# Kernel optimization log

Hardware: AMD Instinct MI355X
Metric: run time of the kernel (lower is better)

## Reference

```python
import jax, jax.numpy as jnp
import numpy as np

N = 100000   # nodes
E = 1600000  # edges (avg degree 16)
IN_F = 256
OUT_F = 128


def setup_inputs() -> dict:
    key = jax.random.key(0)
    k1, k2, k3, k4, k5, k6 = jax.random.split(key, 6)
    std = 1.0 / (OUT_F ** 0.5)
    return {
        "x": jax.random.normal(k1, (N, IN_F), dtype=jnp.float32),
        "weight": jax.random.uniform(k2, (IN_F, OUT_F), dtype=jnp.float32, minval=-std, maxval=std),
        "bias": jax.random.uniform(k3, (OUT_F,), dtype=jnp.float32, minval=-std, maxval=std),
        "edge_weight": jax.random.uniform(k4, (E,), dtype=jnp.float32),
        "row": jax.random.randint(k5, (E,), 0, N, dtype=jnp.int32),
        "col": jax.random.randint(k6, (E,), 0, N, dtype=jnp.int32),
    }


def reference(x, weight, bias, edge_weight, row, col):
    # support = x @ W : dense GEMM [N, in] x [in, out]
    support = jnp.matmul(x, weight)
    # spmm(adj, support): gather source-node rows, scale by edge value,
    # scatter-add into destination rows (COO SpMM).
    msgs = support[col] * edge_weight[:, None]          # [E, out]
    aggregated = jax.ops.segment_sum(msgs, row, num_segments=N)  # [N, out]
    return aggregated + bias
```

## Files before the change

kernel.cpp:

```cpp
#include <hip/hip_runtime.h>

#define N_NODES 100000
#define IN_F 256
#define OUT_F 128

#define BKT_SHIFT 6
#define BKT_SIZE (1 << BKT_SHIFT)
#define NBKT ((N_NODES + BKT_SIZE - 1) / BKT_SIZE)
#define SLAB_CAP 2048
#define CHUNK 8192

#define WS_SUP 0
#define WS_SLAB 25600000
#define WS_BSWZ 51300000
#define WS_BCUR 51400000
#define WS_NEEDED 65200016

typedef __attribute__((ext_vector_type(8))) short short8;
typedef __attribute__((ext_vector_type(4))) float f32x4;
typedef __attribute__((ext_vector_type(2))) float f32x2;

__device__ __forceinline__ unsigned short f2bf(float f) {
  unsigned u = __float_as_uint(f);
  unsigned r = (u + 0x7fffu + ((u >> 16) & 1u)) >> 16;
  return (unsigned short)r;
}

__global__ __launch_bounds__(256) void prep_bswz_kernel(
    const float* __restrict__ w, unsigned short* __restrict__ bswz,
    int* __restrict__ bcur) {
  const int tid = blockIdx.x * 256 + threadIdx.x;
  if (tid < NBKT) bcur[tid] = 0;
  const int j = tid & 7;
  const int lane = (tid >> 3) & 63;
  const int nt = (tid >> 9) & 7;
  const int ks = tid >> 12;
  const int k = ks * 32 + ((lane >> 4) * 8) + j;
  const int n = nt * 16 + (lane & 15);
  bswz[tid] = f2bf(w[k * OUT_F + n]);
}

__global__ __launch_bounds__(512, 4) void gemm_mfma_kernel(
    const float* __restrict__ x, const unsigned short* __restrict__ bswz,
    unsigned short* __restrict__ supb) {
  __shared__ unsigned short lb[32768];

  const int t = threadIdx.x;
  {
    const int4* src = (const int4*)bswz;
    int4* dst = (int4*)lb;
#pragma unroll
    for (int i = 0; i < 8; ++i) dst[t + i * 512] = src[t + i * 512];
  }
  __syncthreads();

  const int w = t >> 6;
  const int lane = t & 63;
  const int quad = lane >> 4;
  const int m16 = lane & 15;

  const int row = blockIdx.x * 128 + w * 16 + m16;
  const int rc = row < N_NODES ? row : N_NODES - 1;
  const float* ap = x + (long long)rc * IN_F + quad * 8;
  const short8* bb = (const short8*)lb + lane;

  f32x4 acc[8];
#pragma unroll
  for (int nt = 0; nt < 8; ++nt) acc[nt] = (f32x4){0.f, 0.f, 0.f, 0.f};

  float4 A0[8], A1[8];
#pragma unroll
  for (int p = 0; p < 6; ++p) {
    A0[p] = *(const float4*)(ap + p * 32);
    A1[p] = *(const float4*)(ap + p * 32 + 4);
  }

#pragma unroll
  for (int ks = 0; ks < 8; ++ks) {
    if (ks + 6 < 8) {
      A0[ks + 6] = *(const float4*)(ap + (ks + 6) * 32);
      A1[ks + 6] = *(const float4*)(ap + (ks + 6) * 32 + 4);
    }
    short8 af;
    af[0] = f2bf(A0[ks].x); af[1] = f2bf(A0[ks].y);
    af[2] = f2bf(A0[ks].z); af[3] = f2bf(A0[ks].w);
    af[4] = f2bf(A1[ks].x); af[5] = f2bf(A1[ks].y);
    af[6] = f2bf(A1[ks].z); af[7] = f2bf(A1[ks].w);
#pragma unroll
    for (int nt = 0; nt < 8; ++nt) {
      const short8 bf = bb[(ks * 8 + nt) * 64];
      acc[nt] = __builtin_amdgcn_mfma_f32_16x16x32_bf16(af, bf, acc[nt], 0, 0, 0);
    }
  }

  const int rowbase = blockIdx.x * 128 + w * 16 + quad * 4;
#pragma unroll
  for (int nt = 0; nt < 8; ++nt) {
#pragma unroll
    for (int r = 0; r < 4; ++r) {
      const int gr = rowbase + r;
      if (gr < N_NODES)
        supb[(long long)gr * OUT_F + nt * 16 + m16] = f2bf(acc[nt][r]);
    }
  }
}

__global__ __launch_bounds__(1024) void bucket_fill_kernel(
    const int* __restrict__ row, const int* __restrict__ col,
    const float* __restrict__ ew, int* __restrict__ bcur,
    int2* __restrict__ slab, int E) {
  __shared__ int lcnt[2048];
  __shared__ int sc[2048];
  __shared__ int outb[2048];
  __shared__ int2 stage[CHUNK];
  __shared__ unsigned short bid[CHUNK];

  const int t = threadIdx.x;
  const int e0 = blockIdx.x * CHUNK;
  lcnt[t] = 0;
  lcnt[t + 1024] = 0;
  __syncthreads();

  int myb[8];
  int rank[8];
  int2 pk[8];
#pragma unroll
  for (int k = 0; k < 8; ++k) {
    const int e = e0 + k * 1024 + t;
    myb[k] = -1;
    if (e < E) {
      const int r = row[e];
      const int c = col[e];
      const float wv = ew[e];
      const int b = r >> BKT_SHIFT;
      myb[k] = b;
      pk[k] = make_int2(c | ((r & (BKT_SIZE - 1)) << 17), __float_as_int(wv));
      rank[k] = atomicAdd(&lcnt[b], 1);
    }
  }
  __syncthreads();

  const int v0 = lcnt[t];
  const int v1 = lcnt[t + 1024];
  sc[t] = v0;
  sc[t + 1024] = v1;
  __syncthreads();
  for (int off = 1; off < 1024; off <<= 1) {
    const int w0 = (t >= off) ? sc[t - off] : 0;
    const int w1 = (t >= off) ? sc[1024 + t - off] : 0;
    __syncthreads();
    sc[t] += w0;
    sc[1024 + t] += w1;
    __syncthreads();
  }
  const int tot0 = sc[1023];
  __syncthreads();
  sc[1024 + t] += tot0;
  __syncthreads();
  const int ex0 = sc[t] - v0;
  const int ex1 = sc[1024 + t] - v1;
  if (v0) outb[t] = atomicAdd(&bcur[t], v0);
  if (t + 1024 < NBKT && v1) outb[t + 1024] = atomicAdd(&bcur[t + 1024], v1);
  __syncthreads();
  sc[t] = ex0;
  sc[t + 1024] = ex1;
  __syncthreads();

#pragma unroll
  for (int k = 0; k < 8; ++k) {
    if (myb[k] >= 0) {
      const int p = sc[myb[k]] + rank[k];
      stage[p] = pk[k];
      bid[p] = (unsigned short)myb[k];
    }
  }
  __syncthreads();

  const int total = min(CHUNK, E - e0);
  for (int i = t; i < total; i += 1024) {
    const int b = bid[i];
    const int rel = outb[b] + (i - sc[b]);
    if (rel < SLAB_CAP) slab[(long long)b * SLAB_CAP + rel] = stage[i];
  }
}

__global__ __launch_bounds__(256) void node_gather_kernel(
    const unsigned short* __restrict__ supb, const int2* __restrict__ slab,
    const int* __restrict__ bcur, const float* __restrict__ bias,
    float* __restrict__ out) {
  __shared__ int2 eS[SLAB_CAP];
  __shared__ int hist[BKT_SIZE];
  __shared__ int sbase[BKT_SIZE];
  __shared__ int cur[BKT_SIZE];

  const int t = threadIdx.x;
  const int bk = blockIdx.x;
  const long long sb = (long long)bk * SLAB_CAP;
  int n = bcur[bk];
  n = n > SLAB_CAP ? SLAB_CAP : n;

  const int w = t >> 6;
  const int lane = t & 63;
  const unsigned short* sp = supb + lane * 2;
  const float2 bv = *(const float2*)(bias + lane * 2);

  if (t < BKT_SIZE) hist[t] = 0;
  __syncthreads();
  for (int i = t; i < n; i += 256)
    atomicAdd(&hist[(slab[sb + i].x >> 17) & (BKT_SIZE - 1)], 1);
  __syncthreads();
  int v = 0;
  if (t < BKT_SIZE) { v = hist[t]; sbase[t] = v; }
  __syncthreads();
  for (int off = 1; off < BKT_SIZE; off <<= 1) {
    int add = 0;
    if (t < BKT_SIZE && t >= off) add = sbase[t - off];
    __syncthreads();
    if (t < BKT_SIZE) sbase[t] += add;
    __syncthreads();
  }
  if (t < BKT_SIZE) { sbase[t] -= v; cur[t] = sbase[t]; }
  __syncthreads();
  for (int i = t; i < n; i += 256) {
    const int2 e = slab[sb + i];
    const int lr = (e.x >> 17) & (BKT_SIZE - 1);
    eS[atomicAdd(&cur[lr], 1)] = e;
  }
  __syncthreads();

  for (int k = 0; k < 16; ++k) {
    const int lr0 = w * 16 + k;
    const int node = (bk << BKT_SHIFT) + lr0;
    if (node >= N_NODES) break;
    const int s = sbase[lr0];
    const int e_end = s + hist[lr0];
    float a0 = 0.f, a1 = 0.f, b0 = 0.f, b1 = 0.f;
    float c0 = 0.f, c1 = 0.f, d0 = 0.f, d1 = 0.f;
    float p0 = 0.f, p1 = 0.f, q0 = 0.f, q1 = 0.f;
    float r0 = 0.f, r1 = 0.f, s0 = 0.f, s1 = 0.f;
    int j = s;
    for (; j + 8 <= e_end; j += 8) {
      const int2 E0 = eS[j];     const int2 E1 = eS[j + 1];
      const int2 E2 = eS[j + 2]; const int2 E3 = eS[j + 3];
      const int2 E4 = eS[j + 4]; const int2 E5 = eS[j + 5];
      const int2 E6 = eS[j + 6]; const int2 E7 = eS[j + 7];
      const unsigned u0 = *(const unsigned*)(sp + (long long)(E0.x & 0x1FFFF) * OUT_F);
      const unsigned u1 = *(const unsigned*)(sp + (long long)(E1.x & 0x1FFFF) * OUT_F);
      const unsigned u2 = *(const unsigned*)(sp + (long long)(E2.x & 0x1FFFF) * OUT_F);
      const unsigned u3 = *(const unsigned*)(sp + (long long)(E3.x & 0x1FFFF) * OUT_F);
      const unsigned u4 = *(const unsigned*)(sp + (long long)(E4.x & 0x1FFFF) * OUT_F);
      const unsigned u5 = *(const unsigned*)(sp + (long long)(E5.x & 0x1FFFF) * OUT_F);
      const unsigned u6 = *(const unsigned*)(sp + (long long)(E6.x & 0x1FFFF) * OUT_F);
      const unsigned u7 = *(const unsigned*)(sp + (long long)(E7.x & 0x1FFFF) * OUT_F);
      a0 = fmaf(__uint_as_float(u0 << 16), __int_as_float(E0.y), a0);
      a1 = fmaf(__uint_as_float(u0 & 0xffff0000u), __int_as_float(E0.y), a1);
      b0 = fmaf(__uint_as_float(u1 << 16), __int_as_float(E1.y), b0);
      b1 = fmaf(__uint_as_float(u1 & 0xffff0000u), __int_as_float(E1.y), b1);
      c0 = fmaf(__uint_as_float(u2 << 16), __int_as_float(E2.y), c0);
      c1 = fmaf(__uint_as_float(u2 & 0xffff0000u), __int_as_float(E2.y), c1);
      d0 = fmaf(__uint_as_float(u3 << 16), __int_as_float(E3.y), d0);
      d1 = fmaf(__uint_as_float(u3 & 0xffff0000u), __int_as_float(E3.y), d1);
      p0 = fmaf(__uint_as_float(u4 << 16), __int_as_float(E4.y), p0);
      p1 = fmaf(__uint_as_float(u4 & 0xffff0000u), __int_as_float(E4.y), p1);
      q0 = fmaf(__uint_as_float(u5 << 16), __int_as_float(E5.y), q0);
      q1 = fmaf(__uint_as_float(u5 & 0xffff0000u), __int_as_float(E5.y), q1);
      r0 = fmaf(__uint_as_float(u6 << 16), __int_as_float(E6.y), r0);
      r1 = fmaf(__uint_as_float(u6 & 0xffff0000u), __int_as_float(E6.y), r1);
      s0 = fmaf(__uint_as_float(u7 << 16), __int_as_float(E7.y), s0);
      s1 = fmaf(__uint_as_float(u7 & 0xffff0000u), __int_as_float(E7.y), s1);
    }
    for (; j + 2 <= e_end; j += 2) {
      const int2 E0 = eS[j];
      const int2 E1 = eS[j + 1];
      const unsigned u0 = *(const unsigned*)(sp + (long long)(E0.x & 0x1FFFF) * OUT_F);
      const unsigned u1 = *(const unsigned*)(sp + (long long)(E1.x & 0x1FFFF) * OUT_F);
      a0 = fmaf(__uint_as_float(u0 << 16), __int_as_float(E0.y), a0);
      a1 = fmaf(__uint_as_float(u0 & 0xffff0000u), __int_as_float(E0.y), a1);
      b0 = fmaf(__uint_as_float(u1 << 16), __int_as_float(E1.y), b0);
      b1 = fmaf(__uint_as_float(u1 & 0xffff0000u), __int_as_float(E1.y), b1);
    }
    if (j < e_end) {
      const int2 E0 = eS[j];
      const unsigned u0 = *(const unsigned*)(sp + (long long)(E0.x & 0x1FFFF) * OUT_F);
      a0 = fmaf(__uint_as_float(u0 << 16), __int_as_float(E0.y), a0);
      a1 = fmaf(__uint_as_float(u0 & 0xffff0000u), __int_as_float(E0.y), a1);
    }
    const f32x2 vv = {a0 + b0 + c0 + d0 + p0 + q0 + r0 + s0 + bv.x,
                      a1 + b1 + c1 + d1 + p1 + q1 + r1 + s1 + bv.y};
    __builtin_nontemporal_store(vv, (f32x2*)(out + (long long)node * OUT_F + lane * 2));
  }
}

__global__ __launch_bounds__(256) void bias_init_kernel(
    float* __restrict__ out, const float* __restrict__ bias) {
  const int t = blockIdx.x * blockDim.x + threadIdx.x;
  const int idx = t * 4;
  *(float4*)(out + idx) = *(const float4*)(bias + (idx & (OUT_F - 1)));
}

__global__ __launch_bounds__(256) void scatter_kernel(
    const unsigned short* __restrict__ supb, const float* __restrict__ ew,
    const int* __restrict__ row, const int* __restrict__ col,
    float* __restrict__ out, int E) {
  const long long t = (long long)blockIdx.x * blockDim.x + threadIdx.x;
  const int e = (int)(t >> 6);
  if (e >= E) return;
  const int lane = (int)(t & 63);
  const int c = col[e];
  const int r = row[e];
  const float wv = ew[e];
  const unsigned u = *(const unsigned*)(supb + (long long)c * OUT_F + lane * 2);
  float* o = out + (long long)r * OUT_F + lane * 2;
  atomicAdd(o, __uint_as_float(u << 16) * wv);
  atomicAdd(o + 1, __uint_as_float(u & 0xffff0000u) * wv);
}

extern "C" void kernel_launch(void* const* d_in, const int* in_sizes, int n_in,
                              void* d_out, int out_size, void* d_ws, size_t ws_size,
                              hipStream_t stream) {
  const float* x = (const float*)d_in[0];
  const float* weight = (const float*)d_in[1];
  const float* bias = (const float*)d_in[2];
  const float* edge_weight = (const float*)d_in[3];
  const int* row = (const int*)d_in[4];
  const int* col = (const int*)d_in[5];
  float* out = (float*)d_out;
  const int E = in_sizes[3];

  char* ws = (char*)d_ws;
  unsigned short* supb = (unsigned short*)(ws + WS_SUP);
  unsigned short* bswz = (unsigned short*)(ws + WS_BSWZ);
  int* bcur = (int*)(ws + WS_BCUR);

  prep_bswz_kernel<<<128, 256, 0, stream>>>(weight, bswz, bcur);
  gemm_mfma_kernel<<<(N_NODES + 127) / 128, 512, 0, stream>>>(x, bswz, supb);

  if (ws_size >= (size_t)WS_NEEDED) {
    int2* slab = (int2*)(ws + WS_SLAB);

    bucket_fill_kernel<<<(E + CHUNK - 1) / CHUNK, 1024, 0, stream>>>(
        row, col, edge_weight, bcur, slab, E);
    node_gather_kernel<<<NBKT, 256, 0, stream>>>(supb, slab, bcur, bias, out);
  } else {
    bias_init_kernel<<<(N_NODES * OUT_F / 4) / 256, 256, 0, stream>>>(out, bias);
    scatter_kernel<<<(int)(((long long)E * 64 + 255) / 256), 256, 0, stream>>>(
        supb, edge_weight, row, col, out, E);
  }
}
```

Measured before the change: 268.5 us.

## Fuse weight prep into GEMM, stage A in LDS, shrink bucket chunks, widen gather loads

Removes the separate weight-swizzle kernel: every GEMM block now converts the fp32 weight to bf16 in LDS itself and also stages its x tile as bf16 in LDS before the MFMA loop. The bucket-fill kernel uses smaller 2048-edge chunks with 512 threads and a per-thread four-bucket scan. The node gather splits each wave into two half-waves that read different edges with 8-byte loads, then combines them with a cross-lane shuffle and writes 16-byte stores. The fallback path now recomputes the projection per edge. The cost is a redundant weight conversion in every GEMM block, more LDS per block (lower occupancy), and more global atomics on the bucket counters.

```diff
diff --git a/kernel.cpp b/kernel.cpp
--- a/kernel.cpp
+++ b/kernel.cpp
@@ -8,17 +8,15 @@
 #define BKT_SIZE (1 << BKT_SHIFT)
 #define NBKT ((N_NODES + BKT_SIZE - 1) / BKT_SIZE)
 #define SLAB_CAP 2048
-#define CHUNK 8192
+#define CHUNK 2048
 
 #define WS_SUP 0
 #define WS_SLAB 25600000
-#define WS_BSWZ 51300000
 #define WS_BCUR 51400000
 #define WS_NEEDED 65200016
 
 typedef __attribute__((ext_vector_type(8))) short short8;
 typedef __attribute__((ext_vector_type(4))) float f32x4;
-typedef __attribute__((ext_vector_type(2))) float f32x2;
 
 __device__ __forceinline__ unsigned short f2bf(float f) {
   unsigned u = __float_as_uint(f);
@@ -26,66 +24,63 @@
   return (unsigned short)r;
 }
 
-__global__ __launch_bounds__(256) void prep_bswz_kernel(
-    const float* __restrict__ w, unsigned short* __restrict__ bswz,
-    int* __restrict__ bcur) {
-  const int tid = blockIdx.x * 256 + threadIdx.x;
-  if (tid < NBKT) bcur[tid] = 0;
-  const int j = tid & 7;
-  const int lane = (tid >> 3) & 63;
-  const int nt = (tid >> 9) & 7;
-  const int ks = tid >> 12;
-  const int k = ks * 32 + ((lane >> 4) * 8) + j;
-  const int n = nt * 16 + (lane & 15);
-  bswz[tid] = f2bf(w[k * OUT_F + n]);
-}
-
-__global__ __launch_bounds__(512, 4) void gemm_mfma_kernel(
-    const float* __restrict__ x, const unsigned short* __restrict__ bswz,
-    unsigned short* __restrict__ supb) {
+__global__ __launch_bounds__(512) void gemm_fused_kernel(
+    const float* __restrict__ x, const float* __restrict__ w,
+    unsigned short* __restrict__ supb, int* __restrict__ bcur) {
   __shared__ unsigned short lb[32768];
+  __shared__ unsigned short la[128 * 264];
 
   const int t = threadIdx.x;
+  const int gtid = blockIdx.x * 512 + t;
+  if (gtid < NBKT) bcur[gtid] = 0;
+
+#pragma unroll
+  for (int i = 0; i < 16; ++i) {
+    const int f4 = t + i * 512;
+    const float4 v = *(const float4*)(w + f4 * 4);
+    const int fid = f4 * 4;
+    const int k = fid >> 7;
+    const int nb = fid & 127;
+    const int base = (k >> 5) * 4096 + (nb >> 4) * 512 +
+                     ((((k >> 3) & 3) * 16 + (nb & 15)) * 8) + (k & 7);
+    lb[base] = f2bf(v.x);
+    lb[base + 8] = f2bf(v.y);
+    lb[base + 16] = f2bf(v.z);
+    lb[base + 24] = f2bf(v.w);
+  }
+
   {
-    const int4* src = (const int4*)bswz;
-    int4* dst = (int4*)lb;
-#pragma unroll
-    for (int i = 0; i < 8; ++i) dst[t + i * 512] = src[t + i * 512];
-  }
-  __syncthreads();
-
-  const int w = t >> 6;
+    const long long gbase = (long long)blockIdx.x * 32768;
+    const long long gmax = (long long)N_NODES * IN_F;
+#pragma unroll
+    for (int i = 0; i < 16; ++i) {
+      const int f4 = t + i * 512;
+      long long g = gbase + (long long)f4 * 4;
+      if (g + 4 > gmax) g = 0;
+      const float4 v = *(const float4*)(x + g);
+      const int row = f4 >> 6;
+      const int col = (f4 & 63) * 4;
+      unsigned short* d = la + row * 264 + col;
+      d[0] = f2bf(v.x); d[1] = f2bf(v.y); d[2] = f2bf(v.z); d[3] = f2bf(v.w);
+    }
+  }
+  __syncthreads();
+
+  const int wv = t >> 6;
   const int lane = t & 63;
   const int quad = lane >> 4;
   const int m16 = lane & 15;
 
-  const int row = blockIdx.x * 128 + w * 16 + m16;
-  const int rc = row < N_NODES ? row : N_NODES - 1;
-  const float* ap = x + (long long)rc * IN_F + quad * 8;
   const short8* bb = (const short8*)lb + lane;
+  const unsigned short* arow = la + (wv * 16 + m16) * 264;
 
   f32x4 acc[8];
 #pragma unroll
   for (int nt = 0; nt < 8; ++nt) acc[nt] = (f32x4){0.f, 0.f, 0.f, 0.f};
 
-  float4 A0[8], A1[8];
-#pragma unroll
-  for (int p = 0; p < 6; ++p) {
-    A0[p] = *(const float4*)(ap + p * 32);
-    A1[p] = *(const float4*)(ap + p * 32 + 4);
-  }
-
 #pragma unroll
   for (int ks = 0; ks < 8; ++ks) {
-    if (ks + 6 < 8) {
-      A0[ks + 6] = *(const float4*)(ap + (ks + 6) * 32);
-      A1[ks + 6] = *(const float4*)(ap + (ks + 6) * 32 + 4);
-    }
-    short8 af;
-    af[0] = f2bf(A0[ks].x); af[1] = f2bf(A0[ks].y);
-    af[2] = f2bf(A0[ks].z); af[3] = f2bf(A0[ks].w);
-    af[4] = f2bf(A1[ks].x); af[5] = f2bf(A1[ks].y);
-    af[6] = f2bf(A1[ks].z); af[7] = f2bf(A1[ks].w);
+    const short8 af = *(const short8*)(arow + ks * 32 + quad * 8);
 #pragma unroll
     for (int nt = 0; nt < 8; ++nt) {
       const short8 bf = bb[(ks * 8 + nt) * 64];
@@ -93,7 +88,7 @@
     }
   }
 
-  const int rowbase = blockIdx.x * 128 + w * 16 + quad * 4;
+  const int rowbase = blockIdx.x * 128 + wv * 16 + quad * 4;
 #pragma unroll
   for (int nt = 0; nt < 8; ++nt) {
 #pragma unroll
@@ -105,71 +100,67 @@
   }
 }
 
-__global__ __launch_bounds__(1024) void bucket_fill_kernel(
+__global__ __launch_bounds__(512) void bucket_fill_kernel(
     const int* __restrict__ row, const int* __restrict__ col,
     const float* __restrict__ ew, int* __restrict__ bcur,
     int2* __restrict__ slab, int E) {
   __shared__ int lcnt[2048];
-  __shared__ int sc[2048];
+  __shared__ int bsum[512];
   __shared__ int outb[2048];
   __shared__ int2 stage[CHUNK];
   __shared__ unsigned short bid[CHUNK];
 
   const int t = threadIdx.x;
   const int e0 = blockIdx.x * CHUNK;
-  lcnt[t] = 0;
-  lcnt[t + 1024] = 0;
-  __syncthreads();
-
-  int myb[8];
-  int rank[8];
-  int2 pk[8];
-#pragma unroll
-  for (int k = 0; k < 8; ++k) {
-    const int e = e0 + k * 1024 + t;
+#pragma unroll
+  for (int i = 0; i < 4; ++i) lcnt[t + i * 512] = 0;
+  __syncthreads();
+
+  int myb[4];
+  int rank[4];
+  int2 pk[4];
+#pragma unroll
+  for (int k = 0; k < 4; ++k) {
+    const int e = e0 + k * 512 + t;
     myb[k] = -1;
     if (e < E) {
       const int r = row[e];
       const int c = col[e];
-      const float wv = ew[e];
+      const float wv2 = ew[e];
       const int b = r >> BKT_SHIFT;
       myb[k] = b;
-      pk[k] = make_int2(c | ((r & (BKT_SIZE - 1)) << 17), __float_as_int(wv));
+      pk[k] = make_int2(c | ((r & (BKT_SIZE - 1)) << 17), __float_as_int(wv2));
       rank[k] = atomicAdd(&lcnt[b], 1);
     }
   }
   __syncthreads();
 
-  const int v0 = lcnt[t];
-  const int v1 = lcnt[t + 1024];
-  sc[t] = v0;
-  sc[t + 1024] = v1;
-  __syncthreads();
-  for (int off = 1; off < 1024; off <<= 1) {
-    const int w0 = (t >= off) ? sc[t - off] : 0;
-    const int w1 = (t >= off) ? sc[1024 + t - off] : 0;
+  const int b0 = t * 4;
+  const int s0 = lcnt[b0], s1 = lcnt[b0 + 1], s2 = lcnt[b0 + 2], s3 = lcnt[b0 + 3];
+  const int tsum = s0 + s1 + s2 + s3;
+  bsum[t] = tsum;
+  __syncthreads();
+  for (int off = 1; off < 512; off <<= 1) {
+    const int u = (t >= off) ? bsum[t - off] : 0;
     __syncthreads();
-    sc[t] += w0;
-    sc[1024 + t] += w1;
+    bsum[t] += u;
     __syncthreads();
   }
-  const int tot0 = sc[1023];
-  __syncthreads();
-  sc[1024 + t] += tot0;
-  __syncthreads();
-  const int ex0 = sc[t] - v0;
-  const int ex1 = sc[1024 + t] - v1;
-  if (v0) outb[t] = atomicAdd(&bcur[t], v0);
-  if (t + 1024 < NBKT && v1) outb[t + 1024] = atomicAdd(&bcur[t + 1024], v1);
-  __syncthreads();
-  sc[t] = ex0;
-  sc[t + 1024] = ex1;
-  __syncthreads();
-
-#pragma unroll
-  for (int k = 0; k < 8; ++k) {
+  const int texc = bsum[t] - tsum;
+  if (s0) outb[b0] = atomicAdd(&bcur[b0], s0);
+  if (s1) outb[b0 + 1] = atomicAdd(&bcur[b0 + 1], s1);
+  if (s2) outb[b0 + 2] = atomicAdd(&bcur[b0 + 2], s2);
+  if (s3) outb[b0 + 3] = atomicAdd(&bcur[b0 + 3], s3);
+  lcnt[b0] = texc;
+  lcnt[b0 + 1] = texc + s0;
+  lcnt[b0 + 2] = texc + s0 + s1;
+  lcnt[b0 + 3] = texc + s0 + s1 + s2;
+  __syncthreads();
+
+#pragma unroll
+  for (int k = 0; k < 4; ++k) {
     if (myb[k] >= 0) {
-      const int p = sc[myb[k]] + rank[k];
+      const int p = lcnt[myb[k]] + rank[k];
       stage[p] = pk[k];
       bid[p] = (unsigned short)myb[k];
     }
@@ -177,9 +168,9 @@
   __syncthreads();
 
   const int total = min(CHUNK, E - e0);
-  for (int i = t; i < total; i += 1024) {
+  for (int i = t; i < total; i += 512) {
     const int b = bid[i];
-    const int rel = outb[b] + (i - sc[b]);
+    const int rel = outb[b] + (i - lcnt[b]);
     if (rel < SLAB_CAP) slab[(long long)b * SLAB_CAP + rel] = stage[i];
   }
 }
@@ -199,95 +190,108 @@
   int n = bcur[bk];
   n = n > SLAB_CAP ? SLAB_CAP : n;
 
-  const int w = t >> 6;
+  const int wv = t >> 6;
   const int lane = t & 63;
-  const unsigned short* sp = supb + lane * 2;
-  const float2 bv = *(const float2*)(bias + lane * 2);
+  const int h = lane >> 5;
+  const int l32 = lane & 31;
+  const unsigned short* sp = supb + l32 * 4;
+  const float4 bv = *(const float4*)(bias + l32 * 4);
 
   if (t < BKT_SIZE) hist[t] = 0;
   __syncthreads();
   for (int i = t; i < n; i += 256)
     atomicAdd(&hist[(slab[sb + i].x >> 17) & (BKT_SIZE - 1)], 1);
   __syncthreads();
-  int v = 0;
-  if (t < BKT_SIZE) { v = hist[t]; sbase[t] = v; }
-  __syncthreads();
-  for (int off = 1; off < BKT_SIZE; off <<= 1) {
-    int add = 0;
-    if (t < BKT_SIZE && t >= off) add = sbase[t - off];
-    __syncthreads();
-    if (t < BKT_SIZE) sbase[t] += add;
-    __syncthreads();
-  }
-  if (t < BKT_SIZE) { sbase[t] -= v; cur[t] = sbase[t]; }
+  if (t < 64) {
+    const int v = hist[t];
+    int sc = v;
+#pragma unroll
+    for (int off = 1; off < 64; off <<= 1) {
+      const int u = __shfl_up(sc, off);
+      if (t >= off) sc += u;
+    }
+    sbase[t] = sc - v;
+    cur[t] = sc - v;
+  }
   __syncthreads();
   for (int i = t; i < n; i += 256) {
     const int2 e = slab[sb + i];
-    const int lr = (e.x >> 17) & (BKT_SIZE - 1);
-    eS[atomicAdd(&cur[lr], 1)] = e;
+    eS[atomicAdd(&cur[(e.x >> 17) & (BKT_SIZE - 1)], 1)] = e;
   }
   __syncthreads();
 
   for (int k = 0; k < 16; ++k) {
-    const int lr0 = w * 16 + k;
-    const int node = (bk << BKT_SHIFT) + lr0;
+    const int lr = wv * 16 + k;
+    const int node = (bk << BKT_SHIFT) + lr;
     if (node >= N_NODES) break;
-    const int s = sbase[lr0];
-    const int e_end = s + hist[lr0];
-    float a0 = 0.f, a1 = 0.f, b0 = 0.f, b1 = 0.f;
-    float c0 = 0.f, c1 = 0.f, d0 = 0.f, d1 = 0.f;
-    float p0 = 0.f, p1 = 0.f, q0 = 0.f, q1 = 0.f;
-    float r0 = 0.f, r1 = 0.f, s0 = 0.f, s1 = 0.f;
+    const int s = sbase[lr];
+    const int e_end = s + hist[lr];
+    float f0 = 0.f, f1 = 0.f, f2 = 0.f, f3 = 0.f;
+    float g0 = 0.f, g1 = 0.f, g2 = 0.f, g3 = 0.f;
+    float p0 = 0.f, p1 = 0.f, p2 = 0.f, p3 = 0.f;
+    float q0 = 0.f, q1 = 0.f, q2 = 0.f, q3 = 0.f;
     int j = s;
     for (; j + 8 <= e_end; j += 8) {
-      const int2 E0 = eS[j];     const int2 E1 = eS[j + 1];
-      const int2 E2 = eS[j + 2]; const int2 E3 = eS[j + 3];
-      const int2 E4 = eS[j + 4]; const int2 E5 = eS[j + 5];
-      const int2 E6 = eS[j + 6]; const int2 E7 = eS[j + 7];
-      const unsigned u0 = *(const unsigned*)(sp + (long long)(E0.x & 0x1FFFF) * OUT_F);
-      const unsigned u1 = *(const unsigned*)(sp + (long long)(E1.x & 0x1FFFF) * OUT_F);
-      const unsigned u2 = *(const unsigned*)(sp + (long long)(E2.x & 0x1FFFF) * OUT_F);
-      const unsigned u3 = *(const unsigned*)(sp + (long long)(E3.x & 0x1FFFF) * OUT_F);
-      const unsigned u4 = *(const unsigned*)(sp + (long long)(E4.x & 0x1FFFF) * OUT_F);
-      const unsigned u5 = *(const unsigned*)(sp + (long long)(E5.x & 0x1FFFF) * OUT_F);
-      const unsigned u6 = *(const unsigned*)(sp + (long long)(E6.x & 0x1FFFF) * OUT_F);
-      const unsigned u7 = *(const unsigned*)(sp + (long long)(E7.x & 0x1FFFF) * OUT_F);
-      a0 = fmaf(__uint_as_float(u0 << 16), __int_as_float(E0.y), a0);
-      a1 = fmaf(__uint_as_float(u0 & 0xffff0000u), __int_as_float(E0.y), a1);
-      b0 = fmaf(__uint_as_float(u1 << 16), __int_as_float(E1.y), b0);
-      b1 = fmaf(__uint_as_float(u1 & 0xffff0000u), __int_as_float(E1.y), b1);
-      c0 = fmaf(__uint_as_float(u2 << 16), __int_as_float(E2.y), c0);
-      c1 = fmaf(__uint_as_float(u2 & 0xffff0000u), __int_as_float(E2.y), c1);
-      d0 = fmaf(__uint_as_float(u3 << 16), __int_as_float(E3.y), d0);
-      d1 = fmaf(__uint_as_float(u3 & 0xffff0000u), __int_as_float(E3.y), d1);
-      p0 = fmaf(__uint_as_float(u4 << 16), __int_as_float(E4.y), p0);
-      p1 = fmaf(__uint_as_float(u4 & 0xffff0000u), __int_as_float(E4.y), p1);
-      q0 = fmaf(__uint_as_float(u5 << 16), __int_as_float(E5.y), q0);
-      q1 = fmaf(__uint_as_float(u5 & 0xffff0000u), __int_as_float(E5.y), q1);
-      r0 = fmaf(__uint_as_float(u6 << 16), __int_as_float(E6.y), r0);
-      r1 = fmaf(__uint_as_float(u6 & 0xffff0000u), __int_as_float(E6.y), r1);
-      s0 = fmaf(__uint_as_float(u7 << 16), __int_as_float(E7.y), s0);
-      s1 = fmaf(__uint_as_float(u7 & 0xffff0000u), __int_as_float(E7.y), s1);
+      const int2 Ea = eS[j + h];
+      const int2 Eb = eS[j + 2 + h];
+      const int2 Ec = eS[j + 4 + h];
+      const int2 Ed = eS[j + 6 + h];
+      const uint2 ua = *(const uint2*)(sp + (long long)(Ea.x & 0x1FFFF) * OUT_F);
+      const uint2 ub = *(const uint2*)(sp + (long long)(Eb.x & 0x1FFFF) * OUT_F);
+      const uint2 uc = *(const uint2*)(sp + (long long)(Ec.x & 0x1FFFF) * OUT_F);
+      const uint2 ud = *(const uint2*)(sp + (long long)(Ed.x & 0x1FFFF) * OUT_F);
+      const float wa = __int_as_float(Ea.y);
+      const float wb = __int_as_float(Eb.y);
+      const float wc = __int_as_float(Ec.y);
+      const float wd = __int_as_float(Ed.y);
+      f0 = fmaf(__uint_as_float(ua.x << 16), wa, f0);
+      f1 = fmaf(__uint_as_float(ua.x & 0xffff0000u), wa, f1);
+      f2 = fmaf(__uint_as_float(ua.y << 16), wa, f2);
+      f3 = fmaf(__uint_as_float(ua.y & 0xffff0000u), wa, f3);
+      g0 = fmaf(__uint_as_float(ub.x << 16), wb, g0);
+      g1 = fmaf(__uint_as_float(ub.x & 0xffff0000u), wb, g1);
+      g2 = fmaf(__uint_as_float(ub.y << 16), wb, g2);
+      g3 = fmaf(__uint_as_float(ub.y & 0xffff0000u), wb, g3);
+      p0 = fmaf(__uint_as_float(uc.x << 16), wc, p0);
+      p1 = fmaf(__uint_as_float(uc.x & 0xffff0000u), wc, p1);
+      p2 = fmaf(__uint_as_float(uc.y << 16), wc, p2);
+      p3 = fmaf(__uint_as_float(uc.y & 0xffff0000u), wc, p3);
+      q0 = fmaf(__uint_as_float(ud.x << 16), wd, q0);
+      q1 = fmaf(__uint_as_float(ud.x & 0xffff0000u), wd, q1);
+      q2 = fmaf(__uint_as_float(ud.y << 16), wd, q2);
+      q3 = fmaf(__uint_as_float(ud.y & 0xffff0000u), wd, q3);
     }
     for (; j + 2 <= e_end; j += 2) {
-      const int2 E0 = eS[j];
-      const int2 E1 = eS[j + 1];
-      const unsigned u0 = *(const unsigned*)(sp + (long long)(E0.x & 0x1FFFF) * OUT_F);
-      const unsigned u1 = *(const unsigned*)(sp + (long long)(E1.x & 0x1FFFF) * OUT_F);
-      a0 = fmaf(__uint_as_float(u0 << 16), __int_as_float(E0.y), a0);
-      a1 = fmaf(__uint_as_float(u0 & 0xffff0000u), __int_as_float(E0.y), a1);
-      b0 = fmaf(__uint_as_float(u1 << 16), __int_as_float(E1.y), b0);
-      b1 = fmaf(__uint_as_float(u1 & 0xffff0000u), __int_as_float(E1.y), b1);
+      const int2 Ea = eS[j + h];
+      const uint2 ua = *(const uint2*)(sp + (long long)(Ea.x & 0x1FFFF) * OUT_F);
+      const float wa = __int_as_float(Ea.y);
+      f0 = fmaf(__uint_as_float(ua.x << 16), wa, f0);
+      f1 = fmaf(__uint_as_float(ua.x & 0xffff0000u), wa, f1);
+      f2 = fmaf(__uint_as_float(ua.y << 16), wa, f2);
+      f3 = fmaf(__uint_as_float(ua.y & 0xffff0000u), wa, f3);
     }
     if (j < e_end) {
-      const int2 E0 = eS[j];
-      const unsigned u0 = *(const unsigned*)(sp + (long long)(E0.x & 0x1FFFF) * OUT_F);
-      a0 = fmaf(__uint_as_float(u0 << 16), __int_as_float(E0.y), a0);
-      a1 = fmaf(__uint_as_float(u0 & 0xffff0000u), __int_as_float(E0.y), a1);
-    }
-    const f32x2 vv = {a0 + b0 + c0 + d0 + p0 + q0 + r0 + s0 + bv.x,
-                      a1 + b1 + c1 + d1 + p1 + q1 + r1 + s1 + bv.y};
-    __builtin_nontemporal_store(vv, (f32x2*)(out + (long long)node * OUT_F + lane * 2));
+      const int idx = (j + h < e_end) ? j + h : j;
+      const int2 Ea = eS[idx];
+      const float wa = (j + h < e_end) ? __int_as_float(Ea.y) : 0.f;
+      const uint2 ua = *(const uint2*)(sp + (long long)(Ea.x & 0x1FFFF) * OUT_F);
+      f0 = fmaf(__uint_as_float(ua.x << 16), wa, f0);
+      f1 = fmaf(__uint_as_float(ua.x & 0xffff0000u), wa, f1);
+      f2 = fmaf(__uint_as_float(ua.y << 16), wa, f2);
+      f3 = fmaf(__uint_as_float(ua.y & 0xffff0000u), wa, f3);
+    }
+    float r0 = f0 + g0 + p0 + q0;
+    float r1 = f1 + g1 + p1 + q1;
+    float r2 = f2 + g2 + p2 + q2;
+    float r3 = f3 + g3 + p3 + q3;
+    r0 += __shfl_xor(r0, 32);
+    r1 += __shfl_xor(r1, 32);
+    r2 += __shfl_xor(r2, 32);
+    r3 += __shfl_xor(r3, 32);
+    if (h == 0) {
+      const f32x4 vv = {r0 + bv.x, r1 + bv.y, r2 + bv.z, r3 + bv.w};
+      __builtin_nontemporal_store(vv, (f32x4*)(out + (long long)node * OUT_F + l32 * 4));
+    }
   }
 }
 
@@ -298,21 +302,26 @@
   *(float4*)(out + idx) = *(const float4*)(bias + (idx & (OUT_F - 1)));
 }
 
-__global__ __launch_bounds__(256) void scatter_kernel(
-    const unsigned short* __restrict__ supb, const float* __restrict__ ew,
-    const int* __restrict__ row, const int* __restrict__ col,
-    float* __restrict__ out, int E) {
+__global__ __launch_bounds__(256) void scatter_fb_kernel(
+    const float* __restrict__ x, const float* __restrict__ w,
+    const float* __restrict__ ew, const int* __restrict__ row,
+    const int* __restrict__ col, float* __restrict__ out, int E) {
   const long long t = (long long)blockIdx.x * blockDim.x + threadIdx.x;
   const int e = (int)(t >> 6);
   if (e >= E) return;
   const int lane = (int)(t & 63);
   const int c = col[e];
   const int r = row[e];
-  const float wv = ew[e];
-  const unsigned u = *(const unsigned*)(supb + (long long)c * OUT_F + lane * 2);
+  const float wv2 = ew[e];
+  float s0 = 0.f, s1 = 0.f;
+  for (int k = 0; k < IN_F; ++k) {
+    const float xv = x[(long long)c * IN_F + k];
+    s0 = fmaf(xv, w[k * OUT_F + lane * 2], s0);
+    s1 = fmaf(xv, w[k * OUT_F + lane * 2 + 1], s1);
+  }
   float* o = out + (long long)r * OUT_F + lane * 2;
-  atomicAdd(o, __uint_as_float(u << 16) * wv);
-  atomicAdd(o + 1, __uint_as_float(u & 0xffff0000u) * wv);
+  atomicAdd(o, s0 * wv2);
+  atomicAdd(o + 1, s1 * wv2);
 }
 
 extern "C" void kernel_launch(void* const* d_in, const int* in_sizes, int n_in,
@@ -329,21 +338,19 @@
 
   char* ws = (char*)d_ws;
   unsigned short* supb = (unsigned short*)(ws + WS_SUP);
-  unsigned short* bswz = (unsigned short*)(ws + WS_BSWZ);
   int* bcur = (int*)(ws + WS_BCUR);
-
-  prep_bswz_kernel<<<128, 256, 0, stream>>>(weight, bswz, bcur);
-  gemm_mfma_kernel<<<(N_NODES + 127) / 128, 512, 0, stream>>>(x, bswz, supb);
 
   if (ws_size >= (size_t)WS_NEEDED) {
     int2* slab = (int2*)(ws + WS_SLAB);
 
-    bucket_fill_kernel<<<(E + CHUNK - 1) / CHUNK, 1024, 0, stream>>>(
+    gemm_fused_kernel<<<(N_NODES + 127) / 128, 512, 0, stream>>>(x, weight, supb,
+                                                                 bcur);
+    bucket_fill_kernel<<<(E + CHUNK - 1) / CHUNK, 512, 0, stream>>>(
         row, col, edge_weight, bcur, slab, E);
     node_gather_kernel<<<NBKT, 256, 0, stream>>>(supb, slab, bcur, bias, out);
   } else {
     bias_init_kernel<<<(N_NODES * OUT_F / 4) / 256, 256, 0, stream>>>(out, bias);
-    scatter_kernel<<<(int)(((long long)E * 64 + 255) / 256), 256, 0, stream>>>(
-        supb, edge_weight, row, col, out, E);
-  }
-}
+    scatter_fb_kernel<<<(int)(((long long)E * 64 + 255) / 256), 256, 0, stream>>>(
+        x, weight, edge_weight, row, col, out, E);
+  }
+}
```

Result: slower. 337.4 us (+25.7%).
